# Kernel tuning notes

Hardware: AMD Instinct MI355X
Metric: run time of the kernel (lower is better)

The kernel has to match this reference:

```python
import jax, jax.numpy as jnp
import numpy as np

VOCAB = 10000
HID = 256

def setup_inputs() -> dict:
    key = jax.random.key(0)
    ks = jax.random.split(key, 7)
    B, T = 64, 64
    input_data = jax.random.randint(ks[0], (B, T), 0, VOCAB, dtype=jnp.int32)
    targets = jax.random.randint(ks[1], (B, T), 0, VOCAB, dtype=jnp.int32)
    # Xavier-ish scaled params
    E = jax.random.normal(ks[2], (VOCAB, HID), dtype=jnp.float32) * (1.0 / np.sqrt(HID))
    W_lstm = jax.random.normal(ks[3], (2 * HID, 4 * HID), dtype=jnp.float32) * (1.0 / np.sqrt(2 * HID))
    b_lstm = jnp.zeros((4 * HID,), dtype=jnp.float32)
    W_dense = jax.random.normal(ks[4], (HID, VOCAB), dtype=jnp.float32) * (1.0 / np.sqrt(HID))
    b_dense = jnp.zeros((VOCAB,), dtype=jnp.float32)
    return {"input_data": input_data, "targets": targets, "E": E,
            "W_lstm": W_lstm, "b_lstm": b_lstm, "W_dense": W_dense, "b_dense": b_dense}

def lstm_scan(xs, W, b, h0, c0):
    # xs: [T, B, H] time-major. TF LSTMCell: gates = [x,h]@W + b, order i,j,f,o, forget_bias=1.0
    def step(carry, x):
        h, c = carry
        gates = jnp.concatenate([x, h], axis=-1) @ W + b  # [B, 4H]
        i, j, f, o = jnp.split(gates, 4, axis=-1)
        c_new = jax.nn.sigmoid(f + 1.0) * c + jax.nn.sigmoid(i) * jnp.tanh(j)
        h_new = jax.nn.sigmoid(o) * jnp.tanh(c_new)
        return (h_new, c_new), h_new
    (hT, cT), hs = jax.lax.scan(step, (h0, c0), xs)
    return hs, (hT, cT)

def reference(input_data, targets, E, W_lstm, b_lstm, W_dense, b_dense):
    B, T = input_data.shape
    inputs = E[input_data]                       # [B, T, H] embedding lookup (no dropout: eval)
    xs = jnp.transpose(inputs, (1, 0, 2))        # [T, B, H]
    h0 = jnp.zeros((B, HID), dtype=E.dtype)
    c0 = jnp.zeros((B, HID), dtype=E.dtype)
    hs, _ = lstm_scan(xs, W_lstm, b_lstm, h0, c0)  # [T, B, H]
    outputs = jnp.transpose(hs, (1, 0, 2))       # [B, T, H]
    logits = outputs @ W_dense + b_dense         # [B, T, V]
    logp = jax.nn.log_softmax(logits, axis=-1)
    ce = -jnp.take_along_axis(logp, targets[..., None].astype(jnp.int32), axis=-1)[..., 0]  # [B, T]
    perplexity = jnp.exp(ce)                     # elementwise, as in add_loss_op
    return perplexity
```

## Files before the change

kernel.cpp:

```cpp
#include <hip/hip_runtime.h>
#include <math.h>

#define VOCABN 10000
#define HIDN   256
#define GATES  1024
#define BN     64
#define TN     64
#define BT     4096
#define NCT    625

#define HPITCH 264
#define HBUFE  4224
#define WLDS_B 131072
#define SMEMSZ (WLDS_B + 2 * HBUFE * 2)

typedef unsigned int       u32;
typedef unsigned short     u16;
typedef unsigned long long u64;
typedef float v4f __attribute__((ext_vector_type(4)));
typedef short v8s __attribute__((ext_vector_type(8)));

__device__ __forceinline__ float bf2f(u16 u) {
    return __uint_as_float(((u32)u) << 16);
}
__device__ __forceinline__ u16 f2bf(float f) {
    u32 u = __float_as_uint(f);
    u += 0x7FFFu + ((u >> 16) & 1u);
    return (u16)(u >> 16);
}
__device__ __forceinline__ float fast_sigmoid(float x) {
    return __builtin_amdgcn_rcpf(1.0f + __expf(-x));
}
__device__ __forceinline__ float fast_tanh(float x) {
    float e = __expf(-2.0f * fabsf(x));
    float t = (1.0f - e) * __builtin_amdgcn_rcpf(1.0f + e);
    return copysignf(t, x);
}

__device__ __forceinline__ void wfrag_dev(
    const float* __restrict__ src, u16* __restrict__ dst, int ncols, int c,
    int t, u16 lt[HIDN][16])
{
    const float* s = src + (size_t)t * ncols + c * 16;
    #pragma unroll
    for (int j4 = 0; j4 < 4; ++j4) {
        float4 v = *(const float4*)(s + j4 * 4);
        lt[t][j4*4+0] = f2bf(v.x);
        lt[t][j4*4+1] = f2bf(v.y);
        lt[t][j4*4+2] = f2bf(v.z);
        lt[t][j4*4+3] = f2bf(v.w);
    }
    __syncthreads();
    #pragma unroll
    for (int h = 0; h < 2; ++h) {
        int f = t + h * 256;
        int q = f >> 6, l = f & 63;
        int m = l & 15, kb = q * 32 + ((l >> 4) & 3) * 8;
        u32 w[4];
        #pragma unroll
        for (int j = 0; j < 4; ++j)
            w[j] = (u32)lt[kb + 2*j][m] | ((u32)lt[kb + 2*j + 1][m] << 16);
        *(uint4*)(dst + (((size_t)c * 8 + q) * 64 + l) * 8) =
            make_uint4(w[0], w[1], w[2], w[3]);
    }
}

__global__ __launch_bounds__(256) void k_wfrag2(
    const float* __restrict__ W_lstm,
    u16* __restrict__ Wxf, u16* __restrict__ Whf)
{
    __shared__ u16 lt[HIDN][16];
    const int bid = blockIdx.x;
    if (bid < 64)
        wfrag_dev(W_lstm, Wxf, GATES, bid, threadIdx.x, lt);
    else
        wfrag_dev(W_lstm + (size_t)HIDN * GATES, Whf, GATES, bid - 64,
                  threadIdx.x, lt);
}

__global__ __launch_bounds__(256) void k_wfrag3(
    const float* __restrict__ W_lstm,
    const float* __restrict__ W_dense,
    u16* __restrict__ Wxf, u16* __restrict__ Whf, u16* __restrict__ Wf)
{
    __shared__ u16 lt[HIDN][16];
    const int bid = blockIdx.x;
    if (bid < 64)
        wfrag_dev(W_lstm, Wxf, GATES, bid, threadIdx.x, lt);
    else if (bid < 128)
        wfrag_dev(W_lstm + (size_t)HIDN * GATES, Whf, GATES, bid - 64,
                  threadIdx.x, lt);
    else
        wfrag_dev(W_dense, Wf, VOCABN, bid - 128, threadIdx.x, lt);
}

__global__ __launch_bounds__(256) void k_wfrag(
    const float* __restrict__ src,
    u16*         __restrict__ dst,
    int ncols)
{
    __shared__ u16 lt[HIDN][16];
    wfrag_dev(src, dst, ncols, blockIdx.x, threadIdx.x, lt);
}

__global__ __launch_bounds__(256) void k_xgates(
    const int*   __restrict__ idx,
    const float* __restrict__ E,
    const u16*   __restrict__ Wxf,
    const float* __restrict__ bl,
    u64*         __restrict__ gx2)
{
    const int bid = blockIdx.x;
    const int t   = bid >> 2, rg = bid & 3;
    const int tid = threadIdx.x;
    const int w   = tid >> 6, lane = tid & 63;
    const int m   = lane & 15, quad = lane >> 4;

    v8s a[8];
    {
        const float* e = E + (size_t)idx[(rg * 16 + m) * TN + t] * HIDN
                         + quad * 8;
        #pragma unroll
        for (int q = 0; q < 8; ++q) {
            float4 x0 = *(const float4*)(e + q * 32);
            float4 x1 = *(const float4*)(e + q * 32 + 4);
            uint4 t4 = make_uint4(
                (u32)f2bf(x0.x) | ((u32)f2bf(x0.y) << 16),
                (u32)f2bf(x0.z) | ((u32)f2bf(x0.w) << 16),
                (u32)f2bf(x1.x) | ((u32)f2bf(x1.y) << 16),
                (u32)f2bf(x1.z) | ((u32)f2bf(x1.w) << 16));
            a[q] = *(v8s*)&t4;
        }
    }

    for (int i = 0; i < 16; ++i) {
        const int c = 4 * i + w;
        v4f acc = {0.f, 0.f, 0.f, 0.f};
        #pragma unroll
        for (int q = 0; q < 8; ++q) {
            v8s b = *(const v8s*)(Wxf + (((size_t)c * 8 + q) * 64 + lane) * 8);
            acc = __builtin_amdgcn_mfma_f32_16x16x32_bf16(a[q], b, acc, 0, 0, 0);
        }
        const float bv = bl[c * 16 + m];
        u32 lo = (u32)f2bf(acc[0] + bv) | ((u32)f2bf(acc[1] + bv) << 16);
        u32 hi = (u32)f2bf(acc[2] + bv) | ((u32)f2bf(acc[3] + bv) << 16);
        u64 pk = (u64)lo | ((u64)hi << 32);
        const size_t di =
            ((((size_t)t * 4 + rg) * 4 + ((c & 15) >> 2)) * 64 + lane) * 16
            + (c & 3) * 4 + (c >> 4);
        gx2[di] = pk;
    }
}

__global__ __launch_bounds__(512, 2) void k_plstm(
    const u16*   __restrict__ Whf,
    const u64*   __restrict__ gx2,
    u16*         __restrict__ Hb)
{
    extern __shared__ char smem[];
    u16* WgL   = (u16*)smem;
    u16* hbufu = (u16*)(smem + WLDS_B);

    const int tid  = threadIdx.x;
    const int rg   = blockIdx.x;
    const int w    = tid >> 6;
    const int lane = tid & 63;
    const int m    = lane & 15, kq = lane >> 4;
    const int gA   = 2 * w, gB = 2 * w + 1;
    const int uA   = 32 * w + m;
    const int uB   = uA + 16;

    v8s wrA[4][8], wrB[2][8];
    #pragma unroll
    for (int gm = 0; gm < 4; ++gm)
        #pragma unroll
        for (int q = 0; q < 8; ++q)
            wrA[gm][q] = *(const v8s*)(
                Whf + (((size_t)(gm * 16 + gA) * 8 + q) * 64 + lane) * 8);
    #pragma unroll
    for (int gm = 0; gm < 2; ++gm)
        #pragma unroll
        for (int q = 0; q < 8; ++q)
            wrB[gm][q] = *(const v8s*)(
                Whf + (((size_t)(gm * 16 + gB) * 8 + q) * 64 + lane) * 8);
    #pragma unroll
    for (int gm2 = 0; gm2 < 2; ++gm2)
        #pragma unroll
        for (int q = 0; q < 8; ++q)
            *(uint4*)(WgL + (((w * 2 + gm2) * 8 + q) * 64 + lane) * 8) =
                *(const uint4*)(
                    Whf + (((size_t)((gm2 + 2) * 16 + gB) * 8 + q) * 64
                           + lane) * 8);

    {
        u32* hz = (u32*)hbufu;
        for (int i = tid; i < HBUFE; i += 512) hz[i] = 0u;
    }

    float cs[8];
    #pragma unroll
    for (int i = 0; i < 8; ++i) cs[i] = 0.0f;

    __syncthreads();

    const int sbase = 8 * (w & 1);

    for (int t = 0; t < TN; ++t) {
        const u16* hrd = hbufu + (t & 1) * HBUFE;
        u16*       hwr = hbufu + ((t + 1) & 1) * HBUFE;

        u64 gb[8];
        {
            const u64* gp = gx2
                + ((((size_t)t * 4 + rg) * 4 + (w >> 1)) * 64 + lane) * 16
                + sbase;
            #pragma unroll
            for (int j = 0; j < 8; ++j) gb[j] = gp[j];
        }

        v4f eA0 = {0.f,0.f,0.f,0.f}, eA1 = {0.f,0.f,0.f,0.f};
        v4f eA2 = {0.f,0.f,0.f,0.f}, eA3 = {0.f,0.f,0.f,0.f};
        v4f eB0 = {0.f,0.f,0.f,0.f}, eB1 = {0.f,0.f,0.f,0.f};
        v4f eB2 = {0.f,0.f,0.f,0.f}, eB3 = {0.f,0.f,0.f,0.f};

        const u16* abase = hrd + m * HPITCH + kq * 8;
        #pragma unroll
        for (int q = 0; q < 8; ++q) {
            v8s aq = *(const v8s*)(abase + q * 32);
            v8s b2 = *(const v8s*)(WgL + (((w * 2 + 0) * 8 + q) * 64 + lane) * 8);
            v8s b3 = *(const v8s*)(WgL + (((w * 2 + 1) * 8 + q) * 64 + lane) * 8);
            eB2 = __builtin_amdgcn_mfma_f32_16x16x32_bf16(aq, b2, eB2, 0, 0, 0);
            eB3 = __builtin_amdgcn_mfma_f32_16x16x32_bf16(aq, b3, eB3, 0, 0, 0);
            eA0 = __builtin_amdgcn_mfma_f32_16x16x32_bf16(aq, wrA[0][q], eA0, 0, 0, 0);
            eA1 = __builtin_amdgcn_mfma_f32_16x16x32_bf16(aq, wrA[1][q], eA1, 0, 0, 0);
            eA2 = __builtin_amdgcn_mfma_f32_16x16x32_bf16(aq, wrA[2][q], eA2, 0, 0, 0);
            eA3 = __builtin_amdgcn_mfma_f32_16x16x32_bf16(aq, wrA[3][q], eA3, 0, 0, 0);
            eB0 = __builtin_amdgcn_mfma_f32_16x16x32_bf16(aq, wrB[0][q], eB0, 0, 0, 0);
            eB1 = __builtin_amdgcn_mfma_f32_16x16x32_bf16(aq, wrB[1][q], eB1, 0, 0, 0);
        }

        const int rb = rg * 16 + kq * 4;
        #pragma unroll
        for (int r = 0; r < 4; ++r) {
            {
                float xi = bf2f((u16)(gb[0] >> (16 * r)));
                float xj = bf2f((u16)(gb[1] >> (16 * r)));
                float xf = bf2f((u16)(gb[2] >> (16 * r)));
                float xo = bf2f((u16)(gb[3] >> (16 * r)));
                float ig = fast_sigmoid(eA0[r] + xi);
                float jt = fast_tanh   (eA1[r] + xj);
                float fg = fast_sigmoid(eA2[r] + xf + 1.0f);
                float og = fast_sigmoid(eA3[r] + xo);
                float cn = fg * cs[r] + ig * jt;
                cs[r] = cn;
                u16 hv = f2bf(og * fast_tanh(cn));
                hwr[(kq * 4 + r) * HPITCH + uA] = hv;
                Hb[((size_t)(rb + r) * TN + t) * HIDN + uA] = hv;
            }
            {
                float xi = bf2f((u16)(gb[4] >> (16 * r)));
                float xj = bf2f((u16)(gb[5] >> (16 * r)));
                float xf = bf2f((u16)(gb[6] >> (16 * r)));
                float xo = bf2f((u16)(gb[7] >> (16 * r)));
                float ig = fast_sigmoid(eB0[r] + xi);
                float jt = fast_tanh   (eB1[r] + xj);
                float fg = fast_sigmoid(eB2[r] + xf + 1.0f);
                float og = fast_sigmoid(eB3[r] + xo);
                float cn = fg * cs[4 + r] + ig * jt;
                cs[4 + r] = cn;
                u16 hv = f2bf(og * fast_tanh(cn));
                hwr[(kq * 4 + r) * HPITCH + uB] = hv;
                Hb[((size_t)(rb + r) * TN + t) * HIDN + uB] = hv;
            }
        }

        asm volatile("s_waitcnt lgkmcnt(0)" ::: "memory");
        __builtin_amdgcn_s_barrier();
    }
}

__global__ __launch_bounds__(256, 1) void k_dense(
    const u16*   __restrict__ Hb,
    const u16*   __restrict__ Wf,
    const float* __restrict__ bd,
    float*       __restrict__ S)
{
    __shared__ float Sl[64];
    const int bid = blockIdx.x;
    const int hv  = bid & 7;
    const int rg  = bid >> 3;
    const int r0  = rg * 64;
    const int tid = threadIdx.x;
    const int w   = tid >> 6, lane = tid & 63;
    const int m   = lane & 15, kq = lane >> 4;

    if (tid < 64) Sl[tid] = 0.0f;

    v8s a[4][8];
    #pragma unroll
    for (int rt = 0; rt < 4; ++rt) {
        const u16* hrow = Hb + (size_t)(r0 + rt * 16 + m) * HIDN + kq * 8;
        #pragma unroll
        for (int q = 0; q < 8; ++q)
            a[rt][q] = *(const v8s*)(hrow + q * 32);
    }
    __syncthreads();

    float s[4][4] = {{0.f,0.f,0.f,0.f},{0.f,0.f,0.f,0.f},
                     {0.f,0.f,0.f,0.f},{0.f,0.f,0.f,0.f}};
    const int cbeg = (hv * NCT) >> 3;
    const int cend = ((hv + 1) * NCT) >> 3;
    for (int c = cbeg + w; c < cend; c += 4) {
        v4f acc[4] = {{0.f,0.f,0.f,0.f},{0.f,0.f,0.f,0.f},
                      {0.f,0.f,0.f,0.f},{0.f,0.f,0.f,0.f}};
        #pragma unroll
        for (int q = 0; q < 8; ++q) {
            v8s bq = *(const v8s*)(Wf + (((size_t)c * 8 + q) * 64 + lane) * 8);
            #pragma unroll
            for (int rt = 0; rt < 4; ++rt)
                acc[rt] = __builtin_amdgcn_mfma_f32_16x16x32_bf16(
                              a[rt][q], bq, acc[rt], 0, 0, 0);
        }
        const float bv = bd[c * 16 + m];
        #pragma unroll
        for (int rt = 0; rt < 4; ++rt)
            #pragma unroll
            for (int r = 0; r < 4; ++r)
                s[rt][r] += __expf(acc[rt][r] + bv);
    }

    #pragma unroll
    for (int rt = 0; rt < 4; ++rt)
        #pragma unroll
        for (int r = 0; r < 4; ++r)
            atomicAdd(&Sl[rt * 16 + kq * 4 + r], s[rt][r]);
    __syncthreads();
    if (tid < 64) S[(size_t)hv * BT + r0 + tid] = Sl[tid];
}

__global__ __launch_bounds__(256) void k_target(
    const u16*   __restrict__ Hb,
    const u16*   __restrict__ Wf,
    const float* __restrict__ bd,
    const int*   __restrict__ tgt,
    const float* __restrict__ S,
    float*       __restrict__ out)
{
    const int tid = threadIdx.x;
    const int row = blockIdx.x * 8 + (tid >> 5);
    const int t   = tid & 31;
    const int q   = t >> 2, lq = t & 3;
    const int v   = tgt[row];
    const int c   = v >> 4, vm = v & 15;
    const int kb  = q * 32 + lq * 8;

    v8s h  = *(const v8s*)(Hb + (size_t)row * HIDN + kb);
    v8s wv = *(const v8s*)(Wf + (((size_t)c * 8 + q) * 64 + lq * 16 + vm) * 8);
    float acc = 0.0f;
    #pragma unroll
    for (int j = 0; j < 8; ++j)
        acc = fmaf(bf2f((u16)h[j]), bf2f((u16)wv[j]), acc);
    #pragma unroll
    for (int off = 16; off >= 1; off >>= 1)
        acc += __shfl_down(acc, off, 32);
    if (t == 0) {
        float tlv = acc + bd[v];
        float sum = 0.0f;
        #pragma unroll
        for (int p = 0; p < 8; ++p) sum += S[(size_t)p * BT + row];
        out[row] = __expf(__logf(sum) - tlv);
    }
}

extern "C" void kernel_launch(void* const* d_in, const int* in_sizes, int n_in,
                              void* d_out, int out_size, void* d_ws, size_t ws_size,
                              hipStream_t stream) {
    const int*   input   = (const int*)  d_in[0];
    const int*   targets = (const int*)  d_in[1];
    const float* E       = (const float*)d_in[2];
    const float* W_lstm  = (const float*)d_in[3];
    const float* b_lstm  = (const float*)d_in[4];
    const float* W_dense = (const float*)d_in[5];
    const float* b_dense = (const float*)d_in[6];
    float* out = (float*)d_out;

    static bool attr_done = false;
    if (!attr_done) {
        hipFuncSetAttribute((const void*)k_plstm,
                            hipFuncAttributeMaxDynamicSharedMemorySize,
                            SMEMSZ);
        attr_done = true;
    }

    char* ws = (char*)d_ws;
    const bool wide = (ws_size >= ((size_t)25 << 20));

    if (wide) {
        u64*   gx2 = (u64*)ws;
        u16*   Wf  = (u16*)(ws + ((size_t)16 << 20));
        u16*   Hb  = (u16*)(ws + ((size_t)21 << 20) + ((size_t)256 << 10));
        u16*   Whf = (u16*)(ws + ((size_t)23 << 20) + ((size_t)256 << 10));
        u16*   Wxf = (u16*)(ws + ((size_t)23 << 20) + ((size_t)768 << 10));
        float* S   = (float*)(ws + ((size_t)24 << 20) + ((size_t)384 << 10));

        k_wfrag3<<<753,     256, 0, stream>>>(W_lstm, W_dense, Wxf, Whf, Wf);
        k_xgates<<<BT / 16, 256, 0, stream>>>(input, E, Wxf, b_lstm, gx2);
        k_plstm <<<4,       512, SMEMSZ, stream>>>(Whf, gx2, Hb);
        k_dense <<<512,     256, 0, stream>>>(Hb, Wf, b_dense, S);
        k_target<<<BT / 8,  256, 0, stream>>>(Hb, Wf, b_dense, targets, S, out);
    } else {
        u64*   gx2 = (u64*)ws;
        u16*   Wf  = (u16*)ws;
        u16*   Hb  = (u16*)(ws + ((size_t)16 << 20));
        u16*   Whf = (u16*)(ws + ((size_t)18 << 20));
        u16*   Wxf = (u16*)(ws + ((size_t)18 << 20) + ((size_t)512 << 10));
        float* S   = (float*)(ws + ((size_t)19 << 20) + ((size_t)128 << 10));

        k_wfrag2<<<128,     256, 0, stream>>>(W_lstm, Wxf, Whf);
        k_xgates<<<BT / 16, 256, 0, stream>>>(input, E, Wxf, b_lstm, gx2);
        k_plstm <<<4,       512, SMEMSZ, stream>>>(Whf, gx2, Hb);
        k_wfrag <<<NCT,     256, 0, stream>>>(W_dense, Wf, VOCABN);
        k_dense <<<512,     256, 0, stream>>>(Hb, Wf, b_dense, S);
        k_target<<<BT / 8,  256, 0, stream>>>(Hb, Wf, b_dense, targets, S, out);
    }
}
```

Baseline: 388.1 us.

## Split LSTM recurrence into one block per batch row

The recurrent LSTM kernel now launches 64 blocks instead of 4, one per batch row. Each block still runs the full 16-row MFMA tile, but only the 16 lanes that own its row do the gate nonlinearities, update the cell state and write h. Each active lane now handles a single row instead of four, which shortens the serial elementwise tail of every timestep. In exchange, every block redundantly loads the recurrent weights and computes 15 rows of MFMA output that are never used.

```diff
diff --git a/kernel.cpp b/kernel.cpp
--- a/kernel.cpp
+++ b/kernel.cpp
@@ -162,14 +162,19 @@
     u16* hbufu = (u16*)(smem + WLDS_B);
 
     const int tid  = threadIdx.x;
-    const int rg   = blockIdx.x;
+    const int bid  = blockIdx.x;
+    const int rg   = bid >> 4;
+    const int rv   = bid & 15;
+    const int kqv  = rv >> 2;
+    const int rr   = rv & 3;
     const int w    = tid >> 6;
     const int lane = tid & 63;
     const int m    = lane & 15, kq = lane >> 4;
-    const int gA   = 2 * w, gB = 2 * w + 1;
     const int uA   = 32 * w + m;
     const int uB   = uA + 16;
-
+    const bool val = (kq == kqv);
+
+    const int gA = 2 * w, gB = 2 * w + 1;
     v8s wrA[4][8], wrB[2][8];
     #pragma unroll
     for (int gm = 0; gm < 4; ++gm)
@@ -197,23 +202,48 @@
         for (int i = tid; i < HBUFE; i += 512) hz[i] = 0u;
     }
 
-    float cs[8];
-    #pragma unroll
-    for (int i = 0; i < 8; ++i) cs[i] = 0.0f;
-
+    float cA = 0.0f, cB = 0.0f;
     __syncthreads();
 
     const int sbase = 8 * (w & 1);
+
+    #define CPAIR(R)                                                          \
+    {                                                                         \
+        float xiA = bf2f((u16)(gb[0] >> (16 * (R))));                         \
+        float xjA = bf2f((u16)(gb[1] >> (16 * (R))));                         \
+        float xfA = bf2f((u16)(gb[2] >> (16 * (R))));                         \
+        float xoA = bf2f((u16)(gb[3] >> (16 * (R))));                         \
+        float igA = fast_sigmoid(eA0[R] + xiA);                               \
+        float jtA = fast_tanh   (eA1[R] + xjA);                               \
+        float fgA = fast_sigmoid(eA2[R] + xfA + 1.0f);                        \
+        float ogA = fast_sigmoid(eA3[R] + xoA);                               \
+        cA = fgA * cA + igA * jtA;                                            \
+        u16 hA = f2bf(ogA * fast_tanh(cA));                                   \
+        float xiB = bf2f((u16)(gb[4] >> (16 * (R))));                         \
+        float xjB = bf2f((u16)(gb[5] >> (16 * (R))));                         \
+        float xfB = bf2f((u16)(gb[6] >> (16 * (R))));                         \
+        float xoB = bf2f((u16)(gb[7] >> (16 * (R))));                         \
+        float igB = fast_sigmoid(eB0[R] + xiB);                               \
+        float jtB = fast_tanh   (eB1[R] + xjB);                               \
+        float fgB = fast_sigmoid(eB2[R] + xfB + 1.0f);                        \
+        float ogB = fast_sigmoid(eB3[R] + xoB);                               \
+        cB = fgB * cB + igB * jtB;                                            \
+        u16 hB = f2bf(ogB * fast_tanh(cB));                                   \
+        hwr[rv * HPITCH + uA] = hA;                                           \
+        hwr[rv * HPITCH + uB] = hB;                                           \
+        Hb[((size_t)bid * TN + t) * HIDN + uA] = hA;                          \
+        Hb[((size_t)bid * TN + t) * HIDN + uB] = hB;                          \
+    }
 
     for (int t = 0; t < TN; ++t) {
         const u16* hrd = hbufu + (t & 1) * HBUFE;
         u16*       hwr = hbufu + ((t + 1) & 1) * HBUFE;
 
         u64 gb[8];
-        {
+        if (val) {
             const u64* gp = gx2
-                + ((((size_t)t * 4 + rg) * 4 + (w >> 1)) * 64 + lane) * 16
-                + sbase;
+                + ((((size_t)t * 4 + rg) * 4 + (w >> 1)) * 64
+                   + kqv * 16 + m) * 16 + sbase;
             #pragma unroll
             for (int j = 0; j < 8; ++j) gb[j] = gp[j];
         }
@@ -239,44 +269,17 @@
             eB1 = __builtin_amdgcn_mfma_f32_16x16x32_bf16(aq, wrB[1][q], eB1, 0, 0, 0);
         }
 
-        const int rb = rg * 16 + kq * 4;
-        #pragma unroll
-        for (int r = 0; r < 4; ++r) {
-            {
-                float xi = bf2f((u16)(gb[0] >> (16 * r)));
-                float xj = bf2f((u16)(gb[1] >> (16 * r)));
-                float xf = bf2f((u16)(gb[2] >> (16 * r)));
-                float xo = bf2f((u16)(gb[3] >> (16 * r)));
-                float ig = fast_sigmoid(eA0[r] + xi);
-                float jt = fast_tanh   (eA1[r] + xj);
-                float fg = fast_sigmoid(eA2[r] + xf + 1.0f);
-                float og = fast_sigmoid(eA3[r] + xo);
-                float cn = fg * cs[r] + ig * jt;
-                cs[r] = cn;
-                u16 hv = f2bf(og * fast_tanh(cn));
-                hwr[(kq * 4 + r) * HPITCH + uA] = hv;
-                Hb[((size_t)(rb + r) * TN + t) * HIDN + uA] = hv;
-            }
-            {
-                float xi = bf2f((u16)(gb[4] >> (16 * r)));
-                float xj = bf2f((u16)(gb[5] >> (16 * r)));
-                float xf = bf2f((u16)(gb[6] >> (16 * r)));
-                float xo = bf2f((u16)(gb[7] >> (16 * r)));
-                float ig = fast_sigmoid(eB0[r] + xi);
-                float jt = fast_tanh   (eB1[r] + xj);
-                float fg = fast_sigmoid(eB2[r] + xf + 1.0f);
-                float og = fast_sigmoid(eB3[r] + xo);
-                float cn = fg * cs[4 + r] + ig * jt;
-                cs[4 + r] = cn;
-                u16 hv = f2bf(og * fast_tanh(cn));
-                hwr[(kq * 4 + r) * HPITCH + uB] = hv;
-                Hb[((size_t)(rb + r) * TN + t) * HIDN + uB] = hv;
-            }
+        if (val) {
+            if      (rr == 0) CPAIR(0)
+            else if (rr == 1) CPAIR(1)
+            else if (rr == 2) CPAIR(2)
+            else              CPAIR(3)
         }
 
         asm volatile("s_waitcnt lgkmcnt(0)" ::: "memory");
         __builtin_amdgcn_s_barrier();
     }
+    #undef CPAIR
 }
 
 __global__ __launch_bounds__(256, 1) void k_dense(
@@ -405,7 +408,7 @@
 
         k_wfrag3<<<753,     256, 0, stream>>>(W_lstm, W_dense, Wxf, Whf, Wf);
         k_xgates<<<BT / 16, 256, 0, stream>>>(input, E, Wxf, b_lstm, gx2);
-        k_plstm <<<4,       512, SMEMSZ, stream>>>(Whf, gx2, Hb);
+        k_plstm <<<64,      512, SMEMSZ, stream>>>(Whf, gx2, Hb);
         k_dense <<<512,     256, 0, stream>>>(Hb, Wf, b_dense, S);
         k_target<<<BT / 8,  256, 0, stream>>>(Hb, Wf, b_dense, targets, S, out);
     } else {
@@ -418,7 +421,7 @@
 
         k_wfrag2<<<128,     256, 0, stream>>>(W_lstm, Wxf, Whf);
         k_xgates<<<BT / 16, 256, 0, stream>>>(input, E, Wxf, b_lstm, gx2);
-        k_plstm <<<4,       512, SMEMSZ, stream>>>(Whf, gx2, Hb);
+        k_plstm <<<64,      512, SMEMSZ, stream>>>(Whf, gx2, Hb);
         k_wfrag <<<NCT,     256, 0, stream>>>(W_dense, Wf, VOCABN);
         k_dense <<<512,     256, 0, stream>>>(Hb, Wf, b_dense, S);
         k_target<<<BT / 8,  256, 0, stream>>>(Hb, Wf, b_dense, targets, S, out);
```

Result: slower. 450.7 us (+16.1%).
